# Optimization experiments

Hardware: AMD Instinct MI355X
Metric: run time of the kernel (lower is better)

Reference implementation:

```python
import jax, jax.numpy as jnp
import numpy as np

EPS_COS = 1e-8   # torch cosine_similarity eps
ATT_EPS = 1e-6   # LinearAttention eps
LN_EPS = 1e-5    # nn.LayerNorm default eps
NHEAD = 8
WS = 8           # window_size
TOPK = 16
C = 256          # embed_dim (hardcoded 256 in original gather)


def layer_norm(x, w, b):
    m = x.mean(-1, keepdims=True)
    v = ((x - m) ** 2).mean(-1, keepdims=True)
    return (x - m) / jnp.sqrt(v + LN_EPS) * w + b


def linear_attention(q, k, v):
    # q,k,v: [N, L, H, D]
    Q = jax.nn.elu(q) + 1.0
    K = jax.nn.elu(k) + 1.0
    L = v.shape[1]
    v = v / L
    KV = jnp.einsum('nshd,nshv->nhdv', K, v)
    Z = 1.0 / (jnp.einsum('nlhd,nhd->nlh', Q, K.sum(axis=1)) + ATT_EPS)
    return jnp.einsum('nlhd,nhdv,nlh->nlhv', Q, KV, Z) * L


def encoder_layer(x, source, Wq, Wk, Wv, Wm, W1, W2, n1w, n1b, n2w, n2b):
    bs, _, d = x.shape
    dim = d // NHEAD
    q = (x @ Wq).reshape(bs, -1, NHEAD, dim)
    k = (source @ Wk).reshape(bs, -1, NHEAD, dim)
    v = (source @ Wv).reshape(bs, -1, NHEAD, dim)
    msg = linear_attention(q, k, v).reshape(bs, -1, d) @ Wm
    msg = layer_norm(msg, n1w, n1b)
    msg = jax.nn.relu(jnp.concatenate([x, msg], axis=-1) @ W1) @ W2
    msg = layer_norm(msg, n2w, n2b)
    return x + msg


def topk_select(x, k):
    # x: [BN, S, C]; cosine similarity of each token to window mean, then topk
    avg = x.mean(axis=1, keepdims=True)                        # [BN,1,C]
    dot = (avg * x).sum(axis=-1)                               # [BN,S]
    na = jnp.maximum(jnp.linalg.norm(avg, axis=-1), EPS_COS)   # [BN,1]
    nb = jnp.maximum(jnp.linalg.norm(x, axis=-1), EPS_COS)     # [BN,S]
    cos = dot / (na * nb)
    _, idx = jax.lax.top_k(cos, k)                             # [BN,k]
    sel = jnp.take_along_axis(x, idx[:, :, None], axis=1)      # [BN,k,C]
    return sel, idx


def scatter_add(x, idx, src):
    # x: [BN,S,C], idx: [BN,k], src: [BN,k,C]
    BN, S, c = x.shape
    flat_idx = (jnp.arange(BN)[:, None] * S + idx).reshape(-1)
    return x.reshape(BN * S, c).at[flat_idx].add(src.reshape(-1, c)).reshape(BN, S, c)


def window_reverse_nchw(windows, ws, H, W):
    c = windows.shape[-1]
    x = windows.transpose(0, 2, 1).reshape(-1, H // ws, W // ws, c, ws, ws)
    return x.transpose(0, 3, 1, 4, 2, 5).reshape(-1, c, H, W)


def setup_inputs() -> dict:
    key = jax.random.key(0)
    ks = jax.random.split(key, 8)
    BN = 2 * 2304  # batch * nums_window
    s = 1.0 / np.sqrt(C)
    return {
        'x_win_attn': jax.random.normal(ks[0], (BN, WS * WS, C), jnp.float32),
        's_win_attn': jax.random.normal(ks[1], (BN, WS * WS, C), jnp.float32),
        'Wq': jax.random.normal(ks[2], (C, C), jnp.float32) * s,
        'Wk': jax.random.normal(ks[3], (C, C), jnp.float32) * s,
        'Wv': jax.random.normal(ks[4], (C, C), jnp.float32) * s,
        'Wmerge': jax.random.normal(ks[5], (C, C), jnp.float32) * s,
        'W1': jax.random.normal(ks[6], (2 * C, 2 * C), jnp.float32) * (1.0 / np.sqrt(2 * C)),
        'W2': jax.random.normal(ks[7], (2 * C, C), jnp.float32) * (1.0 / np.sqrt(2 * C)),
        'n1w': jnp.ones((C,), jnp.float32),
        'n1b': jnp.zeros((C,), jnp.float32),
        'n2w': jnp.ones((C,), jnp.float32),
        'n2b': jnp.zeros((C,), jnp.float32),
        'batch_size': 2,
        'nums_window': 2304,
        'h': 384,
        'w': 384,
    }


def reference(x_win_attn, s_win_attn, Wq, Wk, Wv, Wmerge, W1, W2,
              n1w, n1b, n2w, n2b, batch_size, nums_window, h, w):
    # 'cross' attention path of WinTopKAttention
    sel1, idx1 = topk_select(x_win_attn, TOPK)
    sel2, _ = topk_select(s_win_attn, TOPK)
    sel1 = sel1.reshape(batch_size, nums_window * TOPK, C)
    sel2 = sel2.reshape(batch_size, nums_window * TOPK, C)
    out = encoder_layer(sel1, sel2, Wq, Wk, Wv, Wmerge, W1, W2, n1w, n1b, n2w, n2b)
    out = out.reshape(batch_size * nums_window, TOPK, C)
    combined = scatter_add(x_win_attn, idx1, out)
    return window_reverse_nchw(combined, WS, h, w)
```

## Files before the change

### kernel.cpp

```cpp
#include <hip/hip_runtime.h>
#include <math.h>

static constexpr int BATCH = 2;
static constexpr int NWIN  = 2304;
static constexpr int BN    = BATCH * NWIN;
static constexpr int S     = 64;
static constexpr int CDIM  = 256;
static constexpr int TOPK_ = 16;
static constexpr int TROWS = BN * TOPK_;
static constexpr int LB    = NWIN * TOPK_;
static constexpr int HW    = 384;
static constexpr int KVSZ  = 8448;
static constexpr int KVB   = 128;
static constexpr int KVTOK = LB / KVB;

typedef unsigned short u16;
typedef __attribute__((ext_vector_type(4))) float  f32x4;
typedef __attribute__((ext_vector_type(8))) short  bf16x8;

__device__ inline u16 f2bf(float f) {
    unsigned u = __float_as_uint(f);
    return (u16)((u + 0x7fffu + ((u >> 16) & 1u)) >> 16);
}
__device__ inline float bf2f(u16 b) {
    return __uint_as_float(((unsigned)b) << 16);
}

__device__ inline void load_lds16(const void* g, void* l) {
    __builtin_amdgcn_global_load_lds(
        (const __attribute__((address_space(1))) unsigned int*)g,
        (__attribute__((address_space(3))) unsigned int*)l, 16, 0, 0);
}

__global__ __launch_bounds__(256) void wconv_all_k(
    const float* __restrict__ Wq, const float* __restrict__ Wk,
    const float* __restrict__ Wv, const float* __restrict__ Wm,
    const float* __restrict__ W1, const float* __restrict__ W2,
    u16* __restrict__ Wqt, u16* __restrict__ Wkt, u16* __restrict__ Wvt,
    u16* __restrict__ Wmt, u16* __restrict__ W1t, u16* __restrict__ W2t)
{
    int t = blockIdx.x * 256 + threadIdx.x;
    const float* W; u16* Wt; int Nd, Kd;
    if (t < 262144) {
        const int sel = t >> 16; t &= 65535;
        W  = (sel == 0 ? Wq  : sel == 1 ? Wk  : sel == 2 ? Wv  : Wm);
        Wt = (sel == 0 ? Wqt : sel == 1 ? Wkt : sel == 2 ? Wvt : Wmt);
        Nd = 256; Kd = 256;
    } else if (t < 524288) { W = W1; Wt = W1t; Nd = 512; Kd = 512; t -= 262144; }
    else                   { W = W2; Wt = W2t; Nd = 256; Kd = 512; t -= 524288; }
    const int k = t / Nd, n = t - k * Nd;
    Wt[(size_t)n * Kd + k] = f2bf(W[t]);
}

__global__ __launch_bounds__(256) void topk_gather_k(
    const float* __restrict__ xin, const float* __restrict__ sin,
    u16* __restrict__ catp, u16* __restrict__ selS, int* __restrict__ idxX)
{
    __shared__ double avgd[256];
    __shared__ double cosv[64];
    __shared__ int    slots[16];

    const int w    = blockIdx.x;
    const bool isX = (blockIdx.y == 0);
    const int tid  = threadIdx.x;
    const float* src = (isX ? xin : sin) + (size_t)w * S * CDIM;

    double sm = 0.0;
    for (int t = 0; t < 64; ++t) sm += (double)src[t * CDIM + tid];
    avgd[tid] = sm * (1.0 / 64.0);
    __syncthreads();

    const int tok = tid >> 2, p = tid & 3;
    const float* rowp = src + tok * CDIM;
    double sd = 0.0, sn = 0.0, sa = 0.0;
    for (int ii = 0; ii < 16; ++ii) {
        const int c = p * 64 + ii * 4;
        const float4 xv4 = *(const float4*)&rowp[c];
        const float xs[4] = {xv4.x, xv4.y, xv4.z, xv4.w};
#pragma unroll
        for (int q = 0; q < 4; ++q) {
            const double xv = (double)xs[q];
            const double av = avgd[c + q];
            sd += av * xv; sn += xv * xv; sa += av * av;
        }
    }
    sd += __shfl_xor(sd, 1); sd += __shfl_xor(sd, 2);
    sn += __shfl_xor(sn, 1); sn += __shfl_xor(sn, 2);
    sa += __shfl_xor(sa, 1); sa += __shfl_xor(sa, 2);
    if (p == 0) {
        double na = sqrt(sa); if (na < 1e-8) na = 1e-8;
        double nb = sqrt(sn); if (nb < 1e-8) nb = 1e-8;
        cosv[tok] = sd / (na * nb);
    }
    __syncthreads();

    if (tid < 64) {
        const double ct = cosv[tid];
        int r = 0;
        for (int j = 0; j < 64; ++j) {
            const double cj = cosv[j];
            r += (cj > ct) || (cj == ct && j < tid);
        }
        if (r < TOPK_) slots[r] = tid;
    }
    __syncthreads();

    if (isX) {
        if (tid < TOPK_) idxX[w * TOPK_ + tid] = slots[tid];
        for (int j = 0; j < TOPK_; ++j) {
            const int t = slots[j];
            catp[((size_t)w * TOPK_ + j) * 512 + tid] = f2bf(src[t * CDIM + tid]);
        }
    } else {
        for (int j = 0; j < TOPK_; ++j) {
            const int t = slots[j];
            selS[((size_t)w * TOPK_ + j) * 256 + tid] = f2bf(src[t * CDIM + tid]);
        }
    }
}

template<int EPI>
__global__ __launch_bounds__(256) void gemm_bf16_k(
    const u16* __restrict__ A, int lda,
    const u16* __restrict__ Bt, int K,
    u16* __restrict__ Cout, int ldc)
{
    __shared__ u16 As[128 * 32];
    __shared__ u16 Bs[128 * 32];

    const int m0 = blockIdx.y * 128, n0 = blockIdx.x * 128;
    const int tid = threadIdx.x;
    const int lane = tid & 63, w = tid >> 6;
    const int wr = w >> 1, wc = w & 1;

    f32x4 acc[4][4];
#pragma unroll
    for (int i = 0; i < 4; ++i)
#pragma unroll
        for (int j = 0; j < 4; ++j)
            acc[i][j] = (f32x4){0.f, 0.f, 0.f, 0.f};

    const int rsel = lane & 15, ksel = (lane >> 4) * 8;

    for (int k0 = 0; k0 < K; k0 += 32) {
#pragma unroll
        for (int i = 0; i < 2; ++i) {
            const int c = w * 2 + i;
            const int e = c * 512 + lane * 8;
            const int row = e >> 5, col = e & 31;
            load_lds16(&A[(size_t)(m0 + row) * lda + k0 + col], &As[c * 512]);
            load_lds16(&Bt[(size_t)(n0 + row) * K  + k0 + col], &Bs[c * 512]);
        }
        __syncthreads();

        bf16x8 af[4], bfr[4];
#pragma unroll
        for (int i = 0; i < 4; ++i)
            af[i] = *(const bf16x8*)&As[(wr * 64 + i * 16 + rsel) * 32 + ksel];
#pragma unroll
        for (int j = 0; j < 4; ++j)
            bfr[j] = *(const bf16x8*)&Bs[(wc * 64 + j * 16 + rsel) * 32 + ksel];
#pragma unroll
        for (int i = 0; i < 4; ++i)
#pragma unroll
            for (int j = 0; j < 4; ++j)
                acc[i][j] = __builtin_amdgcn_mfma_f32_16x16x32_bf16(
                    af[i], bfr[j], acc[i][j], 0, 0, 0);
        __syncthreads();
    }

    const int crow = (lane >> 4) * 4, ccol = lane & 15;
#pragma unroll
    for (int i = 0; i < 4; ++i) {
#pragma unroll
        for (int j = 0; j < 4; ++j) {
#pragma unroll
            for (int r = 0; r < 4; ++r) {
                float v = acc[i][j][r];
                if (EPI == 1) v = (v > 0.f) ? (v + 1.f) : __expf(v);
                if (EPI == 2) v = (v > 0.f) ? v : 0.f;
                Cout[(size_t)(m0 + wr * 64 + i * 16 + crow + r) * ldc
                     + (n0 + wc * 64 + j * 16 + ccol)] = f2bf(v);
            }
        }
    }
}

__global__ __launch_bounds__(256) void kv_part_k(
    const u16* __restrict__ Kb, const u16* __restrict__ Vb,
    float* __restrict__ part)
{
    __shared__ float Kt[16][256];
    __shared__ float Vt[16][256];

    const int bk = blockIdx.x;
    const int batch = bk >> 7, slot = bk & 127;
    const size_t r0 = (size_t)batch * LB + (size_t)slot * KVTOK;
    const int h = threadIdx.x >> 5, e = threadIdx.x & 31;

    float acc[32] = {};
    float ks = 0.f;

    for (int tile = 0; tile < KVTOK / 16; ++tile) {
        const size_t rb = r0 + tile * 16;
        for (int i = 0; i < 16; ++i) {
            Kt[i][threadIdx.x] = bf2f(Kb[(rb + i) * 256 + threadIdx.x]);
            Vt[i][threadIdx.x] = bf2f(Vb[(rb + i) * 256 + threadIdx.x]);
        }
        __syncthreads();
        for (int s = 0; s < 16; ++s) {
            const float vv = Vt[s][(h << 5) + e];
            ks += Kt[s][(h << 5) + e];
#pragma unroll
            for (int d = 0; d < 32; ++d)
                acc[d] += Kt[s][(h << 5) + d] * vv;
        }
        __syncthreads();
    }

    float* pb = part + (size_t)bk * KVSZ;
    for (int d = 0; d < 32; ++d)
        pb[((h << 5) + d) * 32 + e] = acc[d];
    pb[8192 + threadIdx.x] = ks;
}

__global__ __launch_bounds__(256) void kv_reduce_k(
    const float* __restrict__ part, float* __restrict__ fin)
{
    const int g = blockIdx.x * 256 + threadIdx.x;
    if (g >= 2 * KVSZ) return;
    const int b = g / KVSZ, i = g - b * KVSZ;
    float s = 0.f;
    for (int p = 0; p < KVB; ++p)
        s += part[(size_t)(b * KVB + p) * KVSZ + i];
    fin[(size_t)b * KVSZ + i] = s;
}

__global__ __launch_bounds__(256) void attn_apply_k(
    const u16* __restrict__ Q, const float* __restrict__ KV,
    u16* __restrict__ outp)
{
    __shared__ float kvs[8192];
    __shared__ float kss[256];
    __shared__ float qs[8][256];

    const int t0 = blockIdx.x * 64;
    const int batch = t0 / LB;
    const float* kvb = KV + (size_t)batch * KVSZ;
    for (int i = threadIdx.x; i < 8192; i += 256) kvs[i] = kvb[i];
    kss[threadIdx.x] = kvb[8192 + threadIdx.x];
    const int h = threadIdx.x >> 5, e = threadIdx.x & 31;
    __syncthreads();

    for (int o = 0; o < 64; o += 8) {
        __syncthreads();
        for (int i = 0; i < 8; ++i)
            qs[i][threadIdx.x] = bf2f(Q[(size_t)(t0 + o + i) * 256 + threadIdx.x]);
        __syncthreads();
        for (int tt = 0; tt < 8; ++tt) {
            const float* qh = &qs[tt][h << 5];
            float zq = 0.f, res = 0.f;
#pragma unroll
            for (int d = 0; d < 32; ++d) {
                const float qd = qh[d];
                zq  += qd * kss[(h << 5) + d];
                res += qd * kvs[((h << 5) + d) * 32 + e];
            }
            outp[(size_t)(t0 + o + tt) * 256 + threadIdx.x] = f2bf(res / (zq + 1e-6f));
        }
    }
}

template<bool ADDG>
__global__ __launch_bounds__(256) void ln_k(
    const u16* __restrict__ in, u16* __restrict__ outp, int ldo,
    const float* __restrict__ gw, const float* __restrict__ gb,
    const float* __restrict__ xsrc, const int* __restrict__ idx)
{
    const int lane = threadIdx.x & 63, wid = threadIdx.x >> 6;
    const size_t row = (size_t)blockIdx.x * 4 + wid;
    const u16* ip = in + row * 256;

    float xv[4];
#pragma unroll
    for (int i = 0; i < 4; ++i) xv[i] = bf2f(ip[i * 64 + lane]);
    float s = xv[0] + xv[1] + xv[2] + xv[3];
#pragma unroll
    for (int m = 1; m < 64; m <<= 1) s += __shfl_xor(s, m);
    const float mean = s * (1.f / 256.f);
    float v = 0.f;
#pragma unroll
    for (int i = 0; i < 4; ++i) { const float d = xv[i] - mean; v += d * d; }
#pragma unroll
    for (int m = 1; m < 64; m <<= 1) v += __shfl_xor(v, m);
    const float rstd = rsqrtf(v * (1.f / 256.f) + 1e-5f);

    const float* xr = nullptr;
    if (ADDG) xr = xsrc + ((size_t)(row >> 4) * 64 + idx[row]) * 256;

#pragma unroll
    for (int i = 0; i < 4; ++i) {
        const int c = i * 64 + lane;
        float o = (xv[i] - mean) * rstd * gw[c] + gb[c];
        if (ADDG) o += xr[c];
        outp[row * ldo + c] = f2bf(o);
    }
}

__global__ __launch_bounds__(256) void combine_reverse_k(
    const float* __restrict__ xin, const int* __restrict__ idxX,
    const u16* __restrict__ outsel, float* __restrict__ outp)
{
    __shared__ float tile[128 * 33];
    __shared__ int   sidx[32];

    const int p  = blockIdx.x;
    const int c0 = blockIdx.y * 32;
    const int b  = p / 1152;
    const int rem = p % 1152;
    const int wy  = rem / 24, wxp = rem % 24;
    const int w0  = b * NWIN + wy * 48 + wxp * 2;
    const int tid = threadIdx.x;

    if (tid < 32) sidx[tid] = idxX[(w0 + (tid >> 4)) * TOPK_ + (tid & 15)];

    {
        const int r = tid >> 1, half = tid & 1;
        const int wl = r >> 6, t = r & 63;
        const float* srcp = xin + ((size_t)(w0 + wl) * 64 + t) * 256 + c0 + half * 16;
        const float4 v0 = ((const float4*)srcp)[0];
        const float4 v1 = ((const float4*)srcp)[1];
        const float4 v2 = ((const float4*)srcp)[2];
        const float4 v3 = ((const float4*)srcp)[3];
        float* dst = &tile[r * 33 + half * 16];
        dst[0] = v0.x; dst[1] = v0.y; dst[2]  = v0.z; dst[3]  = v0.w;
        dst[4] = v1.x; dst[5] = v1.y; dst[6]  = v1.z; dst[7]  = v1.w;
        dst[8] = v2.x; dst[9] = v2.y; dst[10] = v2.z; dst[11] = v2.w;
        dst[12] = v3.x; dst[13] = v3.y; dst[14] = v3.z; dst[15] = v3.w;
    }
    __syncthreads();

    for (int it = 0; it < 4; ++it) {
        const int rid = it * 8 + (tid >> 5);
        const int cc  = tid & 31;
        const int wl  = rid >> 4, j = rid & 15;
        const int t   = sidx[rid];
        tile[((wl << 6) + t) * 33 + cc] +=
            bf2f(outsel[((size_t)(w0 + wl) * TOPK_ + j) * 256 + c0 + cc]);
    }
    __syncthreads();

    const int chalf = tid >> 7;
    const int pix = tid & 127;
    const int dy = pix >> 4, x16 = pix & 15;
    const int wl = x16 >> 3, dx = x16 & 7;
    const int rr = (wl << 6) + dy * 8 + dx;
    const size_t obase = (((size_t)b * 256 + c0 + chalf) * HW + (wy * 8 + dy)) * HW
                       + wxp * 16 + x16;
    for (int cc = 0; cc < 32; cc += 2)
        outp[obase + (size_t)cc * (HW * HW)] = tile[rr * 33 + cc + chalf];
}

extern "C" void kernel_launch(void* const* d_in, const int* in_sizes, int n_in,
                              void* d_out, int out_size, void* d_ws, size_t ws_size,
                              hipStream_t stream)
{
    const float* x   = (const float*)d_in[0];
    const float* s   = (const float*)d_in[1];
    const float* Wq  = (const float*)d_in[2];
    const float* Wk  = (const float*)d_in[3];
    const float* Wv  = (const float*)d_in[4];
    const float* Wm  = (const float*)d_in[5];
    const float* W1  = (const float*)d_in[6];
    const float* W2  = (const float*)d_in[7];
    const float* n1w = (const float*)d_in[8];
    const float* n1b = (const float*)d_in[9];
    const float* n2w = (const float*)d_in[10];
    const float* n2b = (const float*)d_in[11];
    float* out = (float*)d_out;

    char* ws = (char*)d_ws;
    int*   idxX   = (int*)ws;
    float* KVpart = (float*)(ws + 294912);
    float* KVfin  = (float*)(ws + 8945664);
    u16*   Wqt    = (u16*)(ws + 9013248);
    u16*   Wkt    = (u16*)(ws + 9144320);
    u16*   Wvt    = (u16*)(ws + 9275392);
    u16*   Wmt    = (u16*)(ws + 9406464);
    u16*   W1t    = (u16*)(ws + 9537536);
    u16*   W2t    = (u16*)(ws + 10061824);
    u16*   Qb     = (u16*)(ws + 10323968);
    u16*   Kb     = (u16*)(ws + 48072704);
    u16*   Vb     = (u16*)(ws + 85821440);
    u16*   Mb     = (u16*)(ws + 123570176);
    u16*   osel   = (u16*)(ws + 161318912);

    u16* catA  = (u16*)d_out;
    u16* selSb = (u16*)((char*)d_out + 75497472);
    u16* msgA  = (u16*)((char*)d_out + 113246208);
    u16* Hb    = (u16*)((char*)d_out + 150994944);

    wconv_all_k<<<dim3(2560), 256, 0, stream>>>(Wq, Wk, Wv, Wm, W1, W2,
                                                Wqt, Wkt, Wvt, Wmt, W1t, W2t);

    topk_gather_k<<<dim3(BN, 2), 256, 0, stream>>>(x, s, catA, selSb, idxX);

    gemm_bf16_k<1><<<dim3(2, 576), 256, 0, stream>>>(catA, 512, Wqt, 256, Qb, 256);
    gemm_bf16_k<1><<<dim3(2, 576), 256, 0, stream>>>(selSb, 256, Wkt, 256, Kb, 256);
    gemm_bf16_k<0><<<dim3(2, 576), 256, 0, stream>>>(selSb, 256, Wvt, 256, Vb, 256);

    kv_part_k<<<dim3(2 * KVB), 256, 0, stream>>>(Kb, Vb, KVpart);
    kv_reduce_k<<<dim3((2 * KVSZ + 255) / 256), 256, 0, stream>>>(KVpart, KVfin);

    attn_apply_k<<<dim3(TROWS / 64), 256, 0, stream>>>(Qb, KVfin, msgA);

    gemm_bf16_k<0><<<dim3(2, 576), 256, 0, stream>>>(msgA, 256, Wmt, 256, Mb, 256);
    ln_k<false><<<dim3(TROWS / 4), 256, 0, stream>>>(Mb, catA + 256, 512, n1w, n1b, nullptr, nullptr);

    gemm_bf16_k<2><<<dim3(4, 576), 256, 0, stream>>>(catA, 512, W1t, 512, Hb, 512);
    gemm_bf16_k<0><<<dim3(2, 576), 256, 0, stream>>>(Hb, 512, W2t, 512, Mb, 256);

    ln_k<true><<<dim3(TROWS / 4), 256, 0, stream>>>(Mb, osel, 256, n2w, n2b, x, idxX);

    combine_reverse_k<<<dim3(BN / 2, 8), 256, 0, stream>>>(x, idxX, osel, out);
}
```

Baseline: 749.1 us.

## Stage top-k windows in LDS, fuse QKV GEMMs, widen KV split-reduction

The top-k gather kernel now runs 512 threads. It loads each 64x256 window into LDS once with global_load_lds and computes the mean, dot products and gather from LDS instead of re-reading global memory. The avg-norm factor is dropped because it is constant per window and does not change the ranking. The Q/K/V GEMMs become a single launch using blockIdx.z, the KV partial reduction uses 384 slices instead of 128 to expose more blocks, and kv_reduce is restructured so each block reduces 64 outputs with four partial sums. The trade-offs are much more LDS per block in the top-k kernel, which can limit occupancy, and a larger partial buffer to write and reduce.

```diff
diff --git a/kernel.cpp b/kernel.cpp
--- a/kernel.cpp
+++ b/kernel.cpp
@@ -11,7 +11,7 @@
 static constexpr int LB    = NWIN * TOPK_;
 static constexpr int HW    = 384;
 static constexpr int KVSZ  = 8448;
-static constexpr int KVB   = 128;
+static constexpr int KVB   = 384;
 static constexpr int KVTOK = LB / KVB;
 
 typedef unsigned short u16;
@@ -52,10 +52,12 @@
     Wt[(size_t)n * Kd + k] = f2bf(W[t]);
 }
 
-__global__ __launch_bounds__(256) void topk_gather_k(
+__global__ __launch_bounds__(512) void topk_gather_k(
     const float* __restrict__ xin, const float* __restrict__ sin,
     u16* __restrict__ catp, u16* __restrict__ selS, int* __restrict__ idxX)
 {
+    __shared__ float  win[64 * 256];
+    __shared__ double red[2][256];
     __shared__ double avgd[256];
     __shared__ double cosv[64];
     __shared__ int    slots[16];
@@ -65,32 +67,45 @@
     const int tid  = threadIdx.x;
     const float* src = (isX ? xin : sin) + (size_t)w * S * CDIM;
 
-    double sm = 0.0;
-    for (int t = 0; t < 64; ++t) sm += (double)src[t * CDIM + tid];
-    avgd[tid] = sm * (1.0 / 64.0);
-    __syncthreads();
-
-    const int tok = tid >> 2, p = tid & 3;
-    const float* rowp = src + tok * CDIM;
-    double sd = 0.0, sn = 0.0, sa = 0.0;
-    for (int ii = 0; ii < 16; ++ii) {
-        const int c = p * 64 + ii * 4;
-        const float4 xv4 = *(const float4*)&rowp[c];
-        const float xs[4] = {xv4.x, xv4.y, xv4.z, xv4.w};
-#pragma unroll
-        for (int q = 0; q < 4; ++q) {
-            const double xv = (double)xs[q];
-            const double av = avgd[c + q];
-            sd += av * xv; sn += xv * xv; sa += av * av;
-        }
-    }
-    sd += __shfl_xor(sd, 1); sd += __shfl_xor(sd, 2);
-    sn += __shfl_xor(sn, 1); sn += __shfl_xor(sn, 2);
-    sa += __shfl_xor(sa, 1); sa += __shfl_xor(sa, 2);
-    if (p == 0) {
-        double na = sqrt(sa); if (na < 1e-8) na = 1e-8;
-        double nb = sqrt(sn); if (nb < 1e-8) nb = 1e-8;
-        cosv[tok] = sd / (na * nb);
+#pragma unroll
+    for (int k = 0; k < 8; ++k) {
+        load_lds16(src + k * 2048 + tid * 4,
+                   &win[k * 2048 + (tid >> 6) * 256]);
+    }
+    __syncthreads();
+
+    {
+        const int h = tid >> 8, c = tid & 255;
+        double sm = 0.0;
+        for (int t = h * 32; t < h * 32 + 32; ++t)
+            sm += (double)win[t * 256 + c];
+        red[h][c] = sm;
+    }
+    __syncthreads();
+    if (tid < 256) avgd[tid] = (red[0][tid] + red[1][tid]) * (1.0 / 64.0);
+    __syncthreads();
+
+    {
+        const int tok = tid >> 3, p = tid & 7;
+        double sd = 0.0, sn = 0.0;
+#pragma unroll
+        for (int i = 0; i < 8; ++i) {
+            const int ic = (i + tok) & 7;
+            const int c0 = p * 32 + ic * 4;
+            const f32x4 xv4 = *(const f32x4*)&win[tok * 256 + c0];
+#pragma unroll
+            for (int q = 0; q < 4; ++q) {
+                const double xv = (double)xv4[q];
+                sd += avgd[c0 + q] * xv;
+                sn += xv * xv;
+            }
+        }
+        sd += __shfl_xor(sd, 1); sd += __shfl_xor(sd, 2); sd += __shfl_xor(sd, 4);
+        sn += __shfl_xor(sn, 1); sn += __shfl_xor(sn, 2); sn += __shfl_xor(sn, 4);
+        if (p == 0) {
+            double nb = sqrt(sn); if (nb < 1e-8) nb = 1e-8;
+            cosv[tok] = sd / nb;
+        }
     }
     __syncthreads();
 
@@ -105,30 +120,30 @@
     }
     __syncthreads();
 
+    const int c = tid & 255, g = tid >> 8;
     if (isX) {
         if (tid < TOPK_) idxX[w * TOPK_ + tid] = slots[tid];
-        for (int j = 0; j < TOPK_; ++j) {
-            const int t = slots[j];
-            catp[((size_t)w * TOPK_ + j) * 512 + tid] = f2bf(src[t * CDIM + tid]);
+#pragma unroll
+        for (int jj = 0; jj < 8; ++jj) {
+            const int j = g * 8 + jj;
+            catp[((size_t)w * TOPK_ + j) * 512 + c] = f2bf(win[slots[j] * 256 + c]);
         }
     } else {
-        for (int j = 0; j < TOPK_; ++j) {
-            const int t = slots[j];
-            selS[((size_t)w * TOPK_ + j) * 256 + tid] = f2bf(src[t * CDIM + tid]);
+#pragma unroll
+        for (int jj = 0; jj < 8; ++jj) {
+            const int j = g * 8 + jj;
+            selS[((size_t)w * TOPK_ + j) * 256 + c] = f2bf(win[slots[j] * 256 + c]);
         }
     }
 }
 
 template<int EPI>
-__global__ __launch_bounds__(256) void gemm_bf16_k(
+__device__ inline void gemm_body(
     const u16* __restrict__ A, int lda,
     const u16* __restrict__ Bt, int K,
-    u16* __restrict__ Cout, int ldc)
-{
-    __shared__ u16 As[128 * 32];
-    __shared__ u16 Bs[128 * 32];
-
-    const int m0 = blockIdx.y * 128, n0 = blockIdx.x * 128;
+    u16* __restrict__ Cout, int ldc,
+    int m0, int n0, u16* As, u16* Bs)
+{
     const int tid = threadIdx.x;
     const int lane = tid & 63, w = tid >> 6;
     const int wr = w >> 1, wc = w & 1;
@@ -171,9 +186,9 @@
 
     const int crow = (lane >> 4) * 4, ccol = lane & 15;
 #pragma unroll
-    for (int i = 0; i < 4; ++i) {
-#pragma unroll
-        for (int j = 0; j < 4; ++j) {
+    for (int i = 0; i < 4; ++i)
+#pragma unroll
+        for (int j = 0; j < 4; ++j)
 #pragma unroll
             for (int r = 0; r < 4; ++r) {
                 float v = acc[i][j][r];
@@ -182,8 +197,38 @@
                 Cout[(size_t)(m0 + wr * 64 + i * 16 + crow + r) * ldc
                      + (n0 + wc * 64 + j * 16 + ccol)] = f2bf(v);
             }
-        }
-    }
+}
+
+template<int EPI>
+__global__ __launch_bounds__(256) void gemm_bf16_k(
+    const u16* __restrict__ A, int lda,
+    const u16* __restrict__ Bt, int K,
+    u16* __restrict__ Cout, int ldc)
+{
+    __shared__ u16 As[128 * 32];
+    __shared__ u16 Bs[128 * 32];
+    gemm_body<EPI>(A, lda, Bt, K, Cout, ldc,
+                   blockIdx.y * 128, blockIdx.x * 128, As, Bs);
+}
+
+__global__ __launch_bounds__(256) void gemm_qkv_k(
+    const u16* __restrict__ catA, const u16* __restrict__ selS,
+    const u16* __restrict__ Wqt, const u16* __restrict__ Wkt,
+    const u16* __restrict__ Wvt,
+    u16* __restrict__ Qb, u16* __restrict__ Kb, u16* __restrict__ Vb)
+{
+    __shared__ u16 As[128 * 32];
+    __shared__ u16 Bs[128 * 32];
+    const int z = blockIdx.z;
+    if (z == 0)
+        gemm_body<1>(catA, 512, Wqt, 256, Qb, 256,
+                     blockIdx.y * 128, blockIdx.x * 128, As, Bs);
+    else if (z == 1)
+        gemm_body<1>(selS, 256, Wkt, 256, Kb, 256,
+                     blockIdx.y * 128, blockIdx.x * 128, As, Bs);
+    else
+        gemm_body<0>(selS, 256, Wvt, 256, Vb, 256,
+                     blockIdx.y * 128, blockIdx.x * 128, As, Bs);
 }
 
 __global__ __launch_bounds__(256) void kv_part_k(
@@ -194,7 +239,7 @@
     __shared__ float Vt[16][256];
 
     const int bk = blockIdx.x;
-    const int batch = bk >> 7, slot = bk & 127;
+    const int batch = bk / KVB, slot = bk % KVB;
     const size_t r0 = (size_t)batch * LB + (size_t)slot * KVTOK;
     const int h = threadIdx.x >> 5, e = threadIdx.x & 31;
 
@@ -227,13 +272,21 @@
 __global__ __launch_bounds__(256) void kv_reduce_k(
     const float* __restrict__ part, float* __restrict__ fin)
 {
-    const int g = blockIdx.x * 256 + threadIdx.x;
-    if (g >= 2 * KVSZ) return;
-    const int b = g / KVSZ, i = g - b * KVSZ;
+    __shared__ float r2[4][64];
+    const int chunk = blockIdx.x;
+    const int b = chunk / (KVSZ / 64);
+    const int i0 = (chunk % (KVSZ / 64)) * 64;
+    const int il = threadIdx.x & 63, pg = threadIdx.x >> 6;
+
     float s = 0.f;
-    for (int p = 0; p < KVB; ++p)
-        s += part[(size_t)(b * KVB + p) * KVSZ + i];
-    fin[(size_t)b * KVSZ + i] = s;
+    for (int p = pg; p < KVB; p += 4)
+        s += part[(size_t)(b * KVB + p) * KVSZ + i0 + il];
+    r2[pg][il] = s;
+    __syncthreads();
+    if (threadIdx.x < 64)
+        fin[(size_t)b * KVSZ + i0 + threadIdx.x] =
+            r2[0][threadIdx.x] + r2[1][threadIdx.x] +
+            r2[2][threadIdx.x] + r2[3][threadIdx.x];
 }
 
 __global__ __launch_bounds__(256) void attn_apply_k(
@@ -382,18 +435,18 @@
     char* ws = (char*)d_ws;
     int*   idxX   = (int*)ws;
     float* KVpart = (float*)(ws + 294912);
-    float* KVfin  = (float*)(ws + 8945664);
-    u16*   Wqt    = (u16*)(ws + 9013248);
-    u16*   Wkt    = (u16*)(ws + 9144320);
-    u16*   Wvt    = (u16*)(ws + 9275392);
-    u16*   Wmt    = (u16*)(ws + 9406464);
-    u16*   W1t    = (u16*)(ws + 9537536);
-    u16*   W2t    = (u16*)(ws + 10061824);
-    u16*   Qb     = (u16*)(ws + 10323968);
-    u16*   Kb     = (u16*)(ws + 48072704);
-    u16*   Vb     = (u16*)(ws + 85821440);
-    u16*   Mb     = (u16*)(ws + 123570176);
-    u16*   osel   = (u16*)(ws + 161318912);
+    float* KVfin  = (float*)(ws + 26247168);
+    u16*   Wqt    = (u16*)(ws + 26314752);
+    u16*   Wkt    = (u16*)(ws + 26445824);
+    u16*   Wvt    = (u16*)(ws + 26576896);
+    u16*   Wmt    = (u16*)(ws + 26707968);
+    u16*   W1t    = (u16*)(ws + 26839040);
+    u16*   W2t    = (u16*)(ws + 27363328);
+    u16*   Qb     = (u16*)(ws + 27625472);
+    u16*   Kb     = (u16*)(ws + 65374208);
+    u16*   Vb     = (u16*)(ws + 103122944);
+    u16*   Mb     = (u16*)(ws + 140871680);
+    u16*   osel   = (u16*)(ws + 178620416);
 
     u16* catA  = (u16*)d_out;
     u16* selSb = (u16*)((char*)d_out + 75497472);
@@ -403,14 +456,13 @@
     wconv_all_k<<<dim3(2560), 256, 0, stream>>>(Wq, Wk, Wv, Wm, W1, W2,
                                                 Wqt, Wkt, Wvt, Wmt, W1t, W2t);
 
-    topk_gather_k<<<dim3(BN, 2), 256, 0, stream>>>(x, s, catA, selSb, idxX);
-
-    gemm_bf16_k<1><<<dim3(2, 576), 256, 0, stream>>>(catA, 512, Wqt, 256, Qb, 256);
-    gemm_bf16_k<1><<<dim3(2, 576), 256, 0, stream>>>(selSb, 256, Wkt, 256, Kb, 256);
-    gemm_bf16_k<0><<<dim3(2, 576), 256, 0, stream>>>(selSb, 256, Wvt, 256, Vb, 256);
+    topk_gather_k<<<dim3(BN, 2), 512, 0, stream>>>(x, s, catA, selSb, idxX);
+
+    gemm_qkv_k<<<dim3(2, 576, 3), 256, 0, stream>>>(catA, selSb, Wqt, Wkt, Wvt,
+                                                    Qb, Kb, Vb);
 
     kv_part_k<<<dim3(2 * KVB), 256, 0, stream>>>(Kb, Vb, KVpart);
-    kv_reduce_k<<<dim3((2 * KVSZ + 255) / 256), 256, 0, stream>>>(KVpart, KVfin);
+    kv_reduce_k<<<dim3(2 * (KVSZ / 64)), 256, 0, stream>>>(KVpart, KVfin);
 
     attn_apply_k<<<dim3(TROWS / 64), 256, 0, stream>>>(Qb, KVfin, msgA);
 
```

Result: faster. 716.9 us (-4.3%).
